# Kernel tuning notes

Measured on AMD Instinct MI355X. Metric: run time of the kernel, lower is better.

The kernel has to match this reference:

```python
import jax, jax.numpy as jnp
import numpy as np

N = 4096      # num_nodes
B = 32        # batch
U = 64        # num_units
L = 2         # num_rnn_layers
K = 2         # max_diffusion_step
OUT = 1       # output_dim (also decoder input_dim)
NM = 2 * K + 1  # num_matrices: 2 supports * K cheb steps + identity


def _random_walk_T(adj):
    # calculate_random_walk_matrix(adj).T : (D^-1 W)^T
    d = adj.sum(axis=1)
    return (adj / d[:, None]).T


def setup_inputs():
    key = jax.random.key(0)
    ks = jax.random.split(key, 16)
    adj = jax.random.uniform(ks[0], (N, N), dtype=jnp.float32)
    S_fwd = _random_walk_T(adj)      # forward transition, transposed
    S_bwd = _random_walk_T(adj.T)    # backward transition, transposed

    inputs = jax.random.normal(ks[1], (B, N, OUT), dtype=jnp.float32)
    hidden_state = jax.random.normal(ks[2], (L, B, N, U), dtype=jnp.float32) * 0.1

    D0 = OUT + U   # layer 0 gconv input width
    D1 = U + U     # layer 1 gconv input width
    s = 0.05
    Wg0 = jax.random.normal(ks[3], (NM * D0, 2 * U), jnp.float32) * s
    bg0 = jnp.ones((2 * U,), jnp.float32)          # bias_start = 1.0 for gates
    Wc0 = jax.random.normal(ks[4], (NM * D0, U), jnp.float32) * s
    bc0 = jnp.zeros((U,), jnp.float32)
    Wg1 = jax.random.normal(ks[5], (NM * D1, 2 * U), jnp.float32) * s
    bg1 = jnp.ones((2 * U,), jnp.float32)
    Wc1 = jax.random.normal(ks[6], (NM * D1, U), jnp.float32) * s
    bc1 = jnp.zeros((U,), jnp.float32)
    Wp = jax.random.normal(ks[7], (U, OUT), jnp.float32) * s
    bp = jnp.zeros((OUT,), jnp.float32)
    return {
        "inputs": inputs, "hidden_state": hidden_state,
        "S_fwd": S_fwd, "S_bwd": S_bwd,
        "Wg0": Wg0, "bg0": bg0, "Wc0": Wc0, "bc0": bc0,
        "Wg1": Wg1, "bg1": bg1, "Wc1": Wc1, "bc1": bc1,
        "Wp": Wp, "bp": bp,
    }


def _gconv(supports, x, h, W, b):
    # diffusion graph convolution with Chebyshev recursion (DCRNN)
    x0 = jnp.concatenate([x, h], axis=-1)      # (B, N, D)
    xs = [x0]
    for S in supports:
        x1 = jnp.einsum('mn,bnd->bmd', S, x0)
        xs.append(x1)
        xk_2, xk_1 = x0, x1
        for _ in range(K - 1):
            x2 = 2.0 * jnp.einsum('mn,bnd->bmd', S, xk_1) - xk_2
            xs.append(x2)
            xk_2, xk_1 = xk_1, x2
    X = jnp.concatenate(xs, axis=-1)           # (B, N, NM*D)
    return X @ W + b


def _dcgru_cell(supports, x, h, Wg, bg, Wc, bc):
    value = jax.nn.sigmoid(_gconv(supports, x, h, Wg, bg))   # (B, N, 2U)
    r, u = jnp.split(value, 2, axis=-1)
    c = jnp.tanh(_gconv(supports, x, r * h, Wc, bc))
    return u * h + (1.0 - u) * c


def reference(inputs, hidden_state, S_fwd, S_bwd,
              Wg0, bg0, Wc0, bc0, Wg1, bg1, Wc1, bc1, Wp, bp):
    supports = (S_fwd, S_bwd)
    layer_params = [(Wg0, bg0, Wc0, bc0), (Wg1, bg1, Wc1, bc1)]
    out = inputs
    new_hidden = []
    for i, (Wg, bg, Wc, bc) in enumerate(layer_params):
        h = _dcgru_cell(supports, out, hidden_state[i], Wg, bg, Wc, bc)
        new_hidden.append(h)
        out = h
    predict = out @ Wp + bp                    # (B, N, OUT)
    return predict, jnp.stack(new_hidden)
```

## Files before the change

### kernel.cpp

```cpp
#include <hip/hip_runtime.h>

typedef unsigned short u16;
typedef unsigned int u32;
typedef unsigned long long u64;
typedef short v8s __attribute__((ext_vector_type(8)));
typedef float v4f __attribute__((ext_vector_type(4)));

#define NN 4096
#define BATCH 32

__device__ __forceinline__ float b2f(u16 u) {
  union { u32 i; float f; } c; c.i = ((u32)u) << 16; return c.f;
}
__device__ __forceinline__ u16 f2b(float f) {
  union { float f; u32 i; } c; c.f = f;
  u32 x = c.i;
  return (u16)((x + 0x7fffu + ((x >> 16) & 1u)) >> 16);
}
__device__ __forceinline__ u32 pk2(float a, float b) {
  return (u32)f2b(a) | ((u32)f2b(b) << 16);
}

typedef const __attribute__((address_space(1))) u32* gp_t;
typedef __attribute__((address_space(3))) u32* lp_t;
__device__ __forceinline__ void gld16(const u16* g, u16* l) {
  __builtin_amdgcn_global_load_lds((gp_t)g, (lp_t)l, 16, 0, 0);
}

#define CBAR() asm volatile("" ::: "memory")
#define BARRIER() do { CBAR(); __builtin_amdgcn_s_barrier(); CBAR(); } while (0)
#define LGKM0() asm volatile("s_waitcnt lgkmcnt(0)" ::: "memory")
#define VMC4() asm volatile("s_waitcnt vmcnt(4)" ::: "memory")
#define VMC0() asm volatile("s_waitcnt vmcnt(0)" ::: "memory")

__global__ __launch_bounds__(256) void cvtS(const float* __restrict__ S,
                                            u16* __restrict__ Sb) {
  const u64 idx = ((u64)blockIdx.x * 256 + threadIdx.x) * 8;
  const float4 a = *(const float4*)(S + idx);
  const float4 b = *(const float4*)(S + idx + 4);
  uint4 o;
  o.x = pk2(a.x, a.y); o.y = pk2(a.z, a.w);
  o.z = pk2(b.x, b.y); o.w = pk2(b.z, b.w);
  *(uint4*)(Sb + idx) = o;
}

__global__ __launch_bounds__(512, 2) void gemm256(const u16* __restrict__ A,
                                                  const u16* __restrict__ B,
                                                  u16* __restrict__ Ct,
                                                  const u16* __restrict__ Xt) {
  __shared__ __align__(16) u16 lds[65536];
  const int t = threadIdx.x;
  const int wave = t >> 6, lane = t & 63;
  const int q = lane >> 4, r16 = lane & 15;
  const int wm = wave >> 2, wn = wave & 3;

  const int nwg = (int)(gridDim.x * gridDim.y);
  const int bid = (int)(blockIdx.y * gridDim.x + blockIdx.x);
  const int swz = (bid & 7) * (nwg >> 3) + (bid >> 3);
  const int m0 = (swz & 15) << 8;
  const int c0 = (swz >> 4) << 8;

  v4f acc[8][4];
  const v4f vz = {0.f, 0.f, 0.f, 0.f};
#pragma unroll
  for (int i = 0; i < 8; ++i)
#pragma unroll
    for (int j = 0; j < 4; ++j) acc[i][j] = vz;

  const int srow = t >> 3;
  const int sslot = ((t & 7) ^ (srow & 7)) << 3;
  const u16* pA = A + (u64)(m0 + srow) * NN + sslot;
  const u16* pB = B + (u64)(c0 + srow) * NN + sslot;
  const u64 rstep = (u64)64 * NN;
  const u64 hstep = (u64)128 * NN;
  u16* lw = lds + (wave << 9);

  const int sw8 = (q ^ (r16 & 7)) << 3;
  const int aBase = (wm << 13) + (r16 << 6) + sw8;
  const int bBase = 16384 + ((wn >> 1) << 13) + ((wn & 1) << 12) + (r16 << 6) + sw8;

  const int NT = NN >> 6;

  gld16(pA, lw);
  gld16(pA + rstep, lw + 4096);
  gld16(pA + hstep, lw + 8192);
  gld16(pA + hstep + rstep, lw + 12288);
  gld16(pB, lw + 16384);
  gld16(pB + rstep, lw + 20480);
  gld16(pB + hstep, lw + 24576);
  gld16(pB + hstep + rstep, lw + 28672);
  gld16(pB + 64, lw + 32768 + 16384);
  gld16(pB + 64 + rstep, lw + 32768 + 20480);
  gld16(pB + 64 + hstep, lw + 32768 + 24576);
  gld16(pB + 64 + hstep + rstep, lw + 32768 + 28672);
  VMC4();
  BARRIER();

  v8s af[4][2], bf01[2][2], bf23[2][2];
#pragma unroll
  for (int i = 0; i < 4; ++i) {
    const int a = aBase + (i << 10);
    af[i][0] = *(const v8s*)(lds + a);
    af[i][1] = *(const v8s*)(lds + (a ^ 32));
  }
#pragma unroll
  for (int j = 0; j < 2; ++j) {
    const int b = bBase + (j << 10);
    bf01[j][0] = *(const v8s*)(lds + b);
    bf01[j][1] = *(const v8s*)(lds + (b ^ 32));
  }

#pragma unroll 2
  for (int T = 0; T < NT; ++T) {
    const int bo = (T & 1) << 15;
    const int no = bo ^ 32768;
    const u64 ka = (u64)(T + 1 < NT ? T + 1 : NT - 1) << 6;
    const u64 kb = (u64)(T + 2 < NT ? T + 2 : NT - 1) << 6;

    gld16(pA + ka, lw + no);
    gld16(pA + ka + rstep, lw + no + 4096);
#pragma unroll
    for (int j = 0; j < 2; ++j) {
      const int b = bo + bBase + ((2 + j) << 10);
      bf23[j][0] = *(const v8s*)(lds + b);
      bf23[j][1] = *(const v8s*)(lds + (b ^ 32));
    }
    __builtin_amdgcn_s_setprio(1);
#pragma unroll
    for (int i = 0; i < 4; ++i)
#pragma unroll
      for (int j = 0; j < 2; ++j) {
        acc[i][j] = __builtin_amdgcn_mfma_f32_16x16x32_bf16(af[i][0], bf01[j][0], acc[i][j], 0, 0, 0);
        acc[i][j] = __builtin_amdgcn_mfma_f32_16x16x32_bf16(af[i][1], bf01[j][1], acc[i][j], 0, 0, 0);
      }
    __builtin_amdgcn_s_setprio(0);

    gld16(pA + hstep + ka, lw + no + 8192);
    gld16(pA + hstep + ka + rstep, lw + no + 12288);
    LGKM0();
    BARRIER();
    __builtin_amdgcn_s_setprio(1);
#pragma unroll
    for (int i = 0; i < 4; ++i)
#pragma unroll
      for (int j = 0; j < 2; ++j) {
        acc[i][2 + j] = __builtin_amdgcn_mfma_f32_16x16x32_bf16(af[i][0], bf23[j][0], acc[i][2 + j], 0, 0, 0);
        acc[i][2 + j] = __builtin_amdgcn_mfma_f32_16x16x32_bf16(af[i][1], bf23[j][1], acc[i][2 + j], 0, 0, 0);
      }
    __builtin_amdgcn_s_setprio(0);
#pragma unroll
    for (int i = 0; i < 4; ++i) {
      const int a = bo + aBase + ((4 + i) << 10);
      af[i][0] = *(const v8s*)(lds + a);
      af[i][1] = *(const v8s*)(lds + (a ^ 32));
    }
    __builtin_amdgcn_sched_barrier(0);

    gld16(pB + kb, lw + bo + 16384);
    gld16(pB + kb + rstep, lw + bo + 20480);
    __builtin_amdgcn_s_setprio(1);
#pragma unroll
    for (int i = 0; i < 4; ++i)
#pragma unroll
      for (int j = 0; j < 2; ++j) {
        acc[4 + i][2 + j] = __builtin_amdgcn_mfma_f32_16x16x32_bf16(af[i][0], bf23[j][0], acc[4 + i][2 + j], 0, 0, 0);
        acc[4 + i][2 + j] = __builtin_amdgcn_mfma_f32_16x16x32_bf16(af[i][1], bf23[j][1], acc[4 + i][2 + j], 0, 0, 0);
      }
    __builtin_amdgcn_s_setprio(0);

    gld16(pB + hstep + kb, lw + bo + 24576);
    gld16(pB + hstep + kb + rstep, lw + bo + 28672);
    VMC4();
    BARRIER();
    __builtin_amdgcn_s_setprio(1);
#pragma unroll
    for (int i = 0; i < 4; ++i)
#pragma unroll
      for (int j = 0; j < 2; ++j) {
        acc[4 + i][j] = __builtin_amdgcn_mfma_f32_16x16x32_bf16(af[i][0], bf01[j][0], acc[4 + i][j], 0, 0, 0);
        acc[4 + i][j] = __builtin_amdgcn_mfma_f32_16x16x32_bf16(af[i][1], bf01[j][1], acc[4 + i][j], 0, 0, 0);
      }
    __builtin_amdgcn_s_setprio(0);
#pragma unroll
    for (int i = 0; i < 4; ++i) {
      const int a = no + aBase + (i << 10);
      af[i][0] = *(const v8s*)(lds + a);
      af[i][1] = *(const v8s*)(lds + (a ^ 32));
    }
#pragma unroll
    for (int j = 0; j < 2; ++j) {
      const int b = no + bBase + (j << 10);
      bf01[j][0] = *(const v8s*)(lds + b);
      bf01[j][1] = *(const v8s*)(lds + (b ^ 32));
    }
    __builtin_amdgcn_sched_barrier(0);
  }

  VMC0();
  __syncthreads();
#pragma unroll
  for (int i = 0; i < 8; ++i)
#pragma unroll
    for (int j = 0; j < 4; ++j) {
      const int cl = (wn << 6) + (j << 4) + r16;
      const int ml = (wm << 7) + (i << 4) + (q << 2);
      const int phys = (cl << 8) + ((((ml >> 3) ^ (cl & 7)) << 3) | (ml & 7));
      uint2 pv;
      pv.x = pk2(acc[i][j][0], acc[i][j][1]);
      pv.y = pk2(acc[i][j][2], acc[i][j][3]);
      *(uint2*)(lds + phys) = pv;
    }
  __syncthreads();
#pragma unroll
  for (int it = 0; it < 16; ++it) {
    const int f = (it << 9) + t;
    const int cl = f >> 5, sl = f & 31;
    const int phys = (cl << 8) + ((sl ^ (cl & 7)) << 3);
    union { uint4 v; u16 e[8]; } tv;
    tv.v = *(const uint4*)(lds + phys);
    const u64 gi = (u64)(c0 + cl) * NN + m0 + (sl << 3);
    if (Xt) {
      union { uint4 v; u16 e[8]; } xv, ov;
      xv.v = *(const uint4*)(Xt + gi);
#pragma unroll
      for (int s = 0; s < 8; ++s) ov.e[s] = f2b(2.f * b2f(tv.e[s]) - b2f(xv.e[s]));
      *(uint4*)(Ct + gi) = ov.v;
    } else {
      *(uint4*)(Ct + gi) = tv.v;
    }
  }
}

__global__ __launch_bounds__(256) void gemm_s(const float* __restrict__ A,
                                              const u16* __restrict__ B,
                                              u16* __restrict__ Ct,
                                              const u16* __restrict__ Xt) {
  __shared__ __align__(16) u16 As[4096];
  __shared__ __align__(16) u16 Bs[4096];
  __shared__ __align__(16) u16 T[16384];
  const int t = threadIdx.x;
  const int wave = t >> 6, lane = t & 63;
  const int m0 = blockIdx.x << 7, c0 = blockIdx.y << 7;
  const int wm = (wave >> 1) << 6, wc = (wave & 1) << 6;
  const int q = lane >> 4, r16 = lane & 15;
  v4f acc[4][4];
  const v4f vz = {0.f, 0.f, 0.f, 0.f};
#pragma unroll
  for (int i = 0; i < 4; ++i)
#pragma unroll
    for (int j = 0; j < 4; ++j) acc[i][j] = vz;

  const int sr = t >> 2;
  const int sc = (t & 3) << 3;
  const u64 abase = (u64)(m0 + sr) * NN + sc;
  const u64 bbase = (u64)(c0 + sr) * NN + sc;
  const u64 rstep = (u64)64 * NN;
  u16* as0 = As + sr * 32 + sc;
  u16* as1 = As + (64 + sr) * 32 + sc;
  u16* bs0 = Bs + sr * 32 + sc;
  u16* bs1 = Bs + (64 + sr) * 32 + sc;

  for (int k0 = 0; k0 < NN; k0 += 32) {
    const float4 a0l = *(const float4*)(A + abase + k0);
    const float4 a0h = *(const float4*)(A + abase + k0 + 4);
    const float4 a1l = *(const float4*)(A + abase + rstep + k0);
    const float4 a1h = *(const float4*)(A + abase + rstep + k0 + 4);
    const uint4 b0 = *(const uint4*)(B + bbase + k0);
    const uint4 b1 = *(const uint4*)(B + bbase + rstep + k0);
    uint4 pa0, pa1;
    pa0.x = pk2(a0l.x, a0l.y); pa0.y = pk2(a0l.z, a0l.w);
    pa0.z = pk2(a0h.x, a0h.y); pa0.w = pk2(a0h.z, a0h.w);
    pa1.x = pk2(a1l.x, a1l.y); pa1.y = pk2(a1l.z, a1l.w);
    pa1.z = pk2(a1h.x, a1h.y); pa1.w = pk2(a1h.z, a1h.w);
    __syncthreads();
    *(uint4*)as0 = pa0;
    *(uint4*)as1 = pa1;
    *(uint4*)bs0 = b0;
    *(uint4*)bs1 = b1;
    __syncthreads();
    v8s af[4], bf[4];
#pragma unroll
    for (int i = 0; i < 4; ++i)
      af[i] = *(const v8s*)(As + ((wm + i * 16 + r16) << 5) + (q << 3));
#pragma unroll
    for (int j = 0; j < 4; ++j)
      bf[j] = *(const v8s*)(Bs + ((wc + j * 16 + r16) << 5) + (q << 3));
#pragma unroll
    for (int i = 0; i < 4; ++i)
#pragma unroll
      for (int j = 0; j < 4; ++j)
        acc[i][j] = __builtin_amdgcn_mfma_f32_16x16x32_bf16(af[i], bf[j], acc[i][j], 0, 0, 0);
  }
#pragma unroll
  for (int i = 0; i < 4; ++i)
#pragma unroll
    for (int j = 0; j < 4; ++j) {
      const int cl = wc + j * 16 + r16;
      const int mm = wm + i * 16 + (q << 2);
      uint2 pv;
      pv.x = pk2(acc[i][j][0], acc[i][j][1]);
      pv.y = pk2(acc[i][j][2], acc[i][j][3]);
      *(uint2*)(T + (cl << 7) + mm) = pv;
    }
  __syncthreads();
#pragma unroll
  for (int it = 0; it < 8; ++it) {
    const int flat = it * 256 + t;
    const int cl = flat >> 4;
    const int seg = (flat & 15) << 3;
    const u64 gi = (u64)(c0 + cl) * NN + m0 + seg;
    union { uint4 v; u16 e[8]; } tv;
    tv.v = *(uint4*)(T + (cl << 7) + seg);
    if (Xt) {
      union { uint4 v; u16 e[8]; } xv, ov;
      xv.v = *(const uint4*)(Xt + gi);
#pragma unroll
      for (int s = 0; s < 8; ++s) ov.e[s] = f2b(2.f * b2f(tv.e[s]) - b2f(xv.e[s]));
      *(uint4*)(Ct + gi) = ov.v;
    } else {
      *(uint4*)(Ct + gi) = tv.v;
    }
  }
}

template <int DP, int KTOT>
__global__ __launch_bounds__(256) void proj_k(const u16* __restrict__ Wt,
                                              const u16* __restrict__ F,
                                              const float* __restrict__ bias,
                                              u16* __restrict__ outp,
                                              const int JSTR, const int ACT) {
  __shared__ __align__(16) u16 As2[2048];
  __shared__ __align__(16) u16 Bs2[4096];
  const int t = threadIdx.x;
  const int wave = t >> 6, lane = t & 63;
  const int q = lane >> 4, r16 = lane & 15;
  const int n0 = blockIdx.x << 7;
  const int j0 = blockIdx.y << 6;
  const int b = blockIdx.z;
  v4f acc[4][2];
  const v4f vz = {0.f, 0.f, 0.f, 0.f};
#pragma unroll
  for (int i = 0; i < 4; ++i) { acc[i][0] = vz; acc[i][1] = vz; }

  const int ar = t >> 2, ac = (t & 3) << 3;
  const u64 wbase = (u64)(j0 + ar) * KTOT + ac;

  for (int k0 = 0; k0 < KTOT; k0 += 32) {
    const uint4 av = *(const uint4*)(Wt + wbase + k0);
    uint4 bv[2];
#pragma unroll
    for (int ci = 0; ci < 2; ++ci) {
      const int c = ci * 256 + t;
      const int kr = c >> 4;
      const int seg = (c & 15) << 3;
      const int kk = k0 + kr;
      const int i = kk / DP;
      const int d = kk - i * DP;
      bv[ci] = *(const uint4*)(F + ((u64)i * (BATCH * DP) + (u64)b * DP + d) * NN + n0 + seg);
    }
    __syncthreads();
    *(uint4*)(As2 + ar * 32 + ac) = av;
#pragma unroll
    for (int ci = 0; ci < 2; ++ci) {
      const int c = ci * 256 + t;
      const int kr = c >> 4;
      const int seg = (c & 15) << 3;
      *(uint4*)(Bs2 + (kr << 7) + seg) = bv[ci];
    }
    __syncthreads();
    v8s af[4], bf[2];
#pragma unroll
    for (int i = 0; i < 4; ++i)
      af[i] = *(const v8s*)(As2 + ((i * 16 + r16) << 5) + (q << 3));
#pragma unroll
    for (int jj = 0; jj < 2; ++jj) {
      const int nn = (wave << 5) + jj * 16 + r16;
      v8s v;
#pragma unroll
      for (int s = 0; s < 8; ++s) v[s] = (short)Bs2[(((q << 3) + s) << 7) + nn];
      bf[jj] = v;
    }
#pragma unroll
    for (int i = 0; i < 4; ++i)
#pragma unroll
      for (int jj = 0; jj < 2; ++jj)
        acc[i][jj] = __builtin_amdgcn_mfma_f32_16x16x32_bf16(af[i], bf[jj], acc[i][jj], 0, 0, 0);
  }
#pragma unroll
  for (int i = 0; i < 4; ++i)
#pragma unroll
    for (int jj = 0; jj < 2; ++jj)
#pragma unroll
      for (int r = 0; r < 4; ++r) {
        const int j = j0 + i * 16 + (q << 2) + r;
        const int n = n0 + (wave << 5) + jj * 16 + r16;
        float v = acc[i][jj][r] + bias[j];
        v = ACT ? (1.f - 2.f / (__expf(2.f * v) + 1.f)) : (1.f / (1.f + __expf(-v)));
        outp[((u64)b * JSTR + j) * NN + n] = f2b(v);
      }
}

__global__ __launch_bounds__(256) void repackW(const float* __restrict__ W, u16* __restrict__ Wt,
                                               const int D, const int DP, const int KTOT,
                                               const int J) {
  const int idx = blockIdx.x * 256 + threadIdx.x;
  if (idx >= J * KTOT) return;
  const int j = idx / KTOT, k = idx - j * KTOT;
  const int i = k / DP, d = k - i * DP;
  u16 v = 0;
  if (i < 5 && d < D) v = f2b(W[(i * D + d) * J + j]);
  Wt[idx] = v;
}

__global__ __launch_bounds__(256) void pack0(const float* __restrict__ x,
                                             const float* __restrict__ hid0,
                                             u16* __restrict__ F0) {
  __shared__ __align__(16) u16 Hs[64 * 72];
  const int b = blockIdx.y, n0 = blockIdx.x << 6, t = threadIdx.x;
  const int r = t >> 2, ds = t & 3;
  const float* hrow = hid0 + ((u64)b * NN + n0 + r) * 64;
#pragma unroll
  for (int c4 = 0; c4 < 4; ++c4) {
    const float4 v = *(const float4*)(hrow + ds * 16 + c4 * 4);
    uint2 p;
    p.x = pk2(v.x, v.y);
    p.y = pk2(v.z, v.w);
    *(uint2*)(Hs + r * 72 + ds * 16 + c4 * 4) = p;
  }
  __syncthreads();
#pragma unroll
  for (int c2 = 0; c2 < 2; ++c2) {
    union { uint4 v; u16 h[8]; } o;
#pragma unroll
    for (int s = 0; s < 8; ++s) o.h[s] = Hs[(ds * 16 + c2 * 8 + s) * 72 + r];
    *(uint4*)(F0 + ((u64)b * 72 + 1 + r) * NN + n0 + ds * 16 + c2 * 8) = o.v;
  }
  if (t < 64) {
    F0[(u64)b * 72 * NN + n0 + t] = f2b(x[(u64)b * NN + n0 + t]);
  } else if (t < 120) {
    const int tt = t - 64;
    const int row = 65 + (tt >> 3), seg = (tt & 7) << 3;
    uint4 z; z.x = z.y = z.z = z.w = 0;
    *(uint4*)(F0 + ((u64)b * 72 + row) * NN + n0 + seg) = z;
  }
}

__global__ __launch_bounds__(256) void pack1(const float* __restrict__ hid1,
                                             u16* __restrict__ F1) {
  __shared__ __align__(16) u16 Hs[64 * 72];
  const int b = blockIdx.y, n0 = blockIdx.x << 6, t = threadIdx.x;
  const int r = t >> 2, ds = t & 3;
  const float* hrow = hid1 + ((u64)b * NN + n0 + r) * 64;
#pragma unroll
  for (int c4 = 0; c4 < 4; ++c4) {
    const float4 v = *(const float4*)(hrow + ds * 16 + c4 * 4);
    uint2 p;
    p.x = pk2(v.x, v.y);
    p.y = pk2(v.z, v.w);
    *(uint2*)(Hs + r * 72 + ds * 16 + c4 * 4) = p;
  }
  __syncthreads();
#pragma unroll
  for (int c2 = 0; c2 < 2; ++c2) {
    union { uint4 v; u16 h[8]; } o;
#pragma unroll
    for (int s = 0; s < 8; ++s) o.h[s] = Hs[(ds * 16 + c2 * 8 + s) * 72 + r];
    *(uint4*)(F1 + ((u64)b * 128 + 64 + r) * NN + n0 + ds * 16 + c2 * 8) = o.v;
  }
}

__global__ __launch_bounds__(256) void candpack(const u16* __restrict__ G, u16* __restrict__ F,
                                                const int DP, const int OFF) {
  const int u = blockIdx.x * 256 + threadIdx.x;
  const int b = u >> 15;
  const int d = (u >> 9) & 63;
  const int seg = (u & 511) << 3;
  union { uint4 v; u16 h[8]; } g, f, o;
  g.v = *(const uint4*)(G + ((u64)b * 128 + d) * NN + seg);
  u16* fp = F + ((u64)b * DP + OFF + d) * NN + seg;
  f.v = *(const uint4*)fp;
#pragma unroll
  for (int s = 0; s < 8; ++s) o.h[s] = f2b(b2f(f.h[s]) * b2f(g.h[s]));
  *(uint4*)fp = o.v;
}

__global__ __launch_bounds__(256) void hnew_k(const u16* __restrict__ G,
                                              const float* __restrict__ hidL,
                                              u16* __restrict__ HnF,
                                              float* __restrict__ outH) {
  __shared__ __align__(16) float Hs[64 * 72];
  __shared__ __align__(16) float T2[64 * 72];
  const int b = blockIdx.y, n0 = blockIdx.x << 6, t = threadIdx.x;
  const int r = t >> 2, ds = t & 3;
  const float* hrow = hidL + ((u64)b * NN + n0 + r) * 64;
#pragma unroll
  for (int c4 = 0; c4 < 4; ++c4)
    *(float4*)(Hs + r * 72 + ds * 16 + c4 * 4) = *(const float4*)(hrow + ds * 16 + c4 * 4);
  __syncthreads();
#pragma unroll
  for (int c2 = 0; c2 < 2; ++c2) {
    const int ncol = ds * 16 + c2 * 8;
    union { uint4 v; u16 h[8]; } uv, cv, o;
    uv.v = *(const uint4*)(G + ((u64)b * 128 + 64 + r) * NN + n0 + ncol);
    cv.v = *(const uint4*)(G + ((u64)b * 128 + r) * NN + n0 + ncol);
#pragma unroll
    for (int s = 0; s < 8; ++s) {
      const int nl = ncol + s;
      const float uu = b2f(uv.h[s]);
      const float hh = Hs[nl * 72 + r];
      const float cc = b2f(cv.h[s]);
      const float v = uu * hh + (1.f - uu) * cc;
      o.h[s] = f2b(v);
      T2[nl * 72 + r] = v;
    }
    *(uint4*)(HnF + ((u64)b * 128 + r) * NN + n0 + ncol) = o.v;
  }
  __syncthreads();
  const int nl2 = t >> 2, dseg = (t & 3) << 4;
#pragma unroll
  for (int c4 = 0; c4 < 4; ++c4) {
    const float4 v = *(const float4*)(T2 + nl2 * 72 + dseg + c4 * 4);
    *(float4*)(outH + ((u64)b * NN + n0 + nl2) * 64 + dseg + c4 * 4) = v;
  }
}

__global__ __launch_bounds__(256) void predictk(const float* __restrict__ H1bnd,
                                                const float* __restrict__ Wp,
                                                const float* __restrict__ bp,
                                                float* __restrict__ outp) {
  __shared__ float w[64];
  __shared__ float bb;
  const int t = threadIdx.x;
  if (t < 64) w[t] = Wp[t];
  if (t == 64) bb = bp[0];
  __syncthreads();
  const int idx = blockIdx.x * 256 + t;
  const float* h = H1bnd + (u64)idx * 64;
  float acc = bb;
#pragma unroll
  for (int c4 = 0; c4 < 16; ++c4) {
    const float4 v = *(const float4*)(h + c4 * 4);
    acc += v.x * w[c4 * 4] + v.y * w[c4 * 4 + 1] + v.z * w[c4 * 4 + 2] + v.w * w[c4 * 4 + 3];
  }
  outp[idx] = acc;
}

static inline void launch_gemm(bool big, const float* Af, const u16* Ab,
                               const u16* B, u16* Ct, const u16* Xt,
                               int Cdim, hipStream_t s) {
  if (big) gemm256<<<dim3(16, Cdim >> 8), 512, 0, s>>>(Ab, B, Ct, Xt);
  else     gemm_s<<<dim3(32, Cdim >> 7), 256, 0, s>>>(Af, B, Ct, Xt);
}

extern "C" void kernel_launch(void* const* d_in, const int* in_sizes, int n_in,
                              void* d_out, int out_size, void* d_ws, size_t ws_size,
                              hipStream_t stream) {
  const float* X   = (const float*)d_in[0];
  const float* HID = (const float*)d_in[1];
  const float* Sf  = (const float*)d_in[2];
  const float* Sb  = (const float*)d_in[3];
  const float* Wg0 = (const float*)d_in[4];
  const float* bg0 = (const float*)d_in[5];
  const float* Wc0 = (const float*)d_in[6];
  const float* bc0 = (const float*)d_in[7];
  const float* Wg1 = (const float*)d_in[8];
  const float* bg1 = (const float*)d_in[9];
  const float* Wc1 = (const float*)d_in[10];
  const float* bc1 = (const float*)d_in[11];
  const float* Wp  = (const float*)d_in[12];
  const float* bp  = (const float*)d_in[13];
  float* OUT = (float*)d_out;
  char* ws = (char*)d_ws;

  u16* F = (u16*)(ws);
  u16* G = (u16*)(ws + 167772160ull);
  const u64 NEED_BIG = 167772160ull + 33554432ull + 2ull * 33554432ull + 393216ull;
  const bool big = ws_size >= NEED_BIG;
  u16* Sfb = (u16*)(ws + 167772160ull + 33554432ull);
  u16* Sbb = Sfb + (u64)NN * NN;
  u16* WT = big ? (Sbb + (u64)NN * NN)
                : (u16*)(ws + 167772160ull + 33554432ull);
  u16* Wg0t = WT;
  u16* Wc0t = Wg0t + 128 * 384;
  u16* Wg1t = Wc0t + 64 * 384;
  u16* Wc1t = Wg1t + 128 * 640;

  const float* HID1 = HID + (u64)32 * 4096 * 64;
  float* OUT_H0 = OUT + 131072;
  float* OUT_H1 = OUT + 131072 + 8388608;

  hipMemsetAsync(ws + (u64)11520 * NN * 2, 0, (u64)2304 * NN * 2, stream);

  if (big) {
    cvtS<<<8192, 256, 0, stream>>>(Sf, Sfb);
    cvtS<<<8192, 256, 0, stream>>>(Sb, Sbb);
  }

  repackW<<<(128 * 384 + 255) / 256, 256, 0, stream>>>(Wg0, Wg0t, 65, 72, 384, 128);
  repackW<<<(64 * 384 + 255) / 256, 256, 0, stream>>>(Wc0, Wc0t, 65, 72, 384, 64);
  repackW<<<(128 * 640 + 255) / 256, 256, 0, stream>>>(Wg1, Wg1t, 128, 128, 640, 128);
  repackW<<<(64 * 640 + 255) / 256, 256, 0, stream>>>(Wc1, Wc1t, 128, 128, 640, 64);

  pack0<<<dim3(64, 32), 256, 0, stream>>>(X, HID, F);
  const u64 R0 = (u64)2304 * NN;
  launch_gemm(big, Sf, Sfb, F, F + R0, nullptr, 2304, stream);
  launch_gemm(big, Sb, Sbb, F, F + 3 * R0, nullptr, 2304, stream);
  launch_gemm(big, Sf, Sfb, F + R0, F + 2 * R0, F, 2304, stream);
  launch_gemm(big, Sb, Sbb, F + 3 * R0, F + 4 * R0, F, 2304, stream);
  proj_k<72, 384><<<dim3(32, 2, 32), 256, 0, stream>>>(Wg0t, F, bg0, G, 128, 0);
  candpack<<<4096, 256, 0, stream>>>(G, F, 72, 1);
  launch_gemm(big, Sf, Sfb, F, F + R0, nullptr, 2304, stream);
  launch_gemm(big, Sb, Sbb, F, F + 3 * R0, nullptr, 2304, stream);
  launch_gemm(big, Sf, Sfb, F + R0, F + 2 * R0, F, 2304, stream);
  launch_gemm(big, Sb, Sbb, F + 3 * R0, F + 4 * R0, F, 2304, stream);
  proj_k<72, 384><<<dim3(32, 1, 32), 256, 0, stream>>>(Wc0t, F, bc0, G, 128, 1);
  hnew_k<<<dim3(64, 32), 256, 0, stream>>>(G, HID, F, OUT_H0);

  pack1<<<dim3(64, 32), 256, 0, stream>>>(HID1, F);
  const u64 R1 = (u64)4096 * NN;
  launch_gemm(big, Sf, Sfb, F, F + R1, nullptr, 4096, stream);
  launch_gemm(big, Sb, Sbb, F, F + 3 * R1, nullptr, 4096, stream);
  launch_gemm(big, Sf, Sfb, F + R1, F + 2 * R1, F, 4096, stream);
  launch_gemm(big, Sb, Sbb, F + 3 * R1, F + 4 * R1, F, 4096, stream);
  proj_k<128, 640><<<dim3(32, 2, 32), 256, 0, stream>>>(Wg1t, F, bg1, G, 128, 0);
  candpack<<<4096, 256, 0, stream>>>(G, F, 128, 64);
  launch_gemm(big, Sf, Sfb, F, F + R1, nullptr, 4096, stream);
  launch_gemm(big, Sb, Sbb, F, F + 3 * R1, nullptr, 4096, stream);
  launch_gemm(big, Sf, Sfb, F + R1, F + 2 * R1, F, 4096, stream);
  launch_gemm(big, Sb, Sbb, F + 3 * R1, F + 4 * R1, F, 4096, stream);
  proj_k<128, 640><<<dim3(32, 1, 32), 256, 0, stream>>>(Wc1t, F, bc1, G, 128, 1);
  hnew_k<<<dim3(64, 32), 256, 0, stream>>>(G, HID1, F, OUT_H1);

  predictk<<<512, 256, 0, stream>>>(OUT_H1, Wp, bp, OUT);
}
```

Measured before the change: 1.991 ms.

## Add 128x256 double-buffered GEMM fusing forward/backward supports for layer 0

Adds a new 512-thread bf16 MFMA GEMM kernel with 128x256 tiles, LDS double buffering with staggered A/B staging, priority hints and workgroup swizzling. It also batches the forward and backward support products into one launch through the z grid dimension. The kernel replaces the four per-layer-0 diffusion GEMM launches with two, cutting launch count and improving reuse and occupancy of the S-matrix tiles. Layer 1 still uses the old path, and the N=2304 column count must divide evenly into 256-wide tiles (9 tiles).

```diff
diff --git a/kernel.cpp b/kernel.cpp
--- a/kernel.cpp
+++ b/kernel.cpp
@@ -227,6 +227,171 @@
       *(uint4*)(Ct + gi) = ov.v;
     } else {
       *(uint4*)(Ct + gi) = tv.v;
+    }
+  }
+}
+
+__global__ __launch_bounds__(512, 2) void gemm_h(const u16* __restrict__ A0f,
+                                                 const u16* __restrict__ A1f,
+                                                 const u16* __restrict__ B0f,
+                                                 const u16* __restrict__ B1f,
+                                                 u16* __restrict__ C0f,
+                                                 u16* __restrict__ C1f,
+                                                 const u16* __restrict__ Xt) {
+  __shared__ __align__(16) u16 lds[49152];
+  const int t = threadIdx.x;
+  const int wave = t >> 6, lane = t & 63;
+  const int q = lane >> 4, r16 = lane & 15;
+  const int wm = wave >> 2, wn = wave & 3;
+  const int z = blockIdx.z;
+  const u16* A = z ? A1f : A0f;
+  const u16* B = z ? B1f : B0f;
+  u16* C = z ? C1f : C0f;
+
+  const int nwg = (int)(gridDim.x * gridDim.y);
+  const int bid = (int)(blockIdx.y * gridDim.x + blockIdx.x);
+  const int swz = (bid & 7) * (nwg >> 3) + (bid >> 3);
+  const int m0 = (swz & 31) << 7;
+  const int c0 = (swz >> 5) << 8;
+
+  v4f acc[4][4];
+  const v4f vz = {0.f, 0.f, 0.f, 0.f};
+#pragma unroll
+  for (int i = 0; i < 4; ++i)
+#pragma unroll
+    for (int j = 0; j < 4; ++j) acc[i][j] = vz;
+
+  const int srow = t >> 3;
+  const int sslot = ((t & 7) ^ (srow & 7)) << 3;
+  const u16* pA = A + (u64)(m0 + srow) * NN + sslot;
+  const u16* pB = B + (u64)(c0 + srow) * NN + sslot;
+  const u64 rstep = (u64)64 * NN;
+  u16* lw = lds + (wave << 9);
+
+  const int sw8 = (q ^ (r16 & 7)) << 3;
+  const int aBase = (wm << 12) + (r16 << 6) + sw8;
+  const int bBase = 8192 + (wn << 12) + (r16 << 6) + sw8;
+
+  const int NT = NN >> 6;
+
+#define STAGE_A(bufo, koff)                        \
+  do {                                             \
+    gld16(pA + (koff), lw + (bufo));               \
+    gld16(pA + rstep + (koff), lw + (bufo) + 4096);\
+  } while (0)
+#define STAGE_B(bufo, koff)                                    \
+  do {                                                         \
+    gld16(pB + (koff), lw + (bufo) + 8192);                    \
+    gld16(pB + rstep + (koff), lw + (bufo) + 12288);           \
+    gld16(pB + 2 * rstep + (koff), lw + (bufo) + 16384);       \
+    gld16(pB + 3 * rstep + (koff), lw + (bufo) + 20480);       \
+  } while (0)
+
+  STAGE_A(0, 0);
+  STAGE_B(0, 0);
+  STAGE_B(24576, 64);
+  VMC4();
+  BARRIER();
+
+  v8s af[4][2], bf01[2][2], bf23[2][2];
+#pragma unroll
+  for (int i = 0; i < 4; ++i) {
+    const int a = aBase + (i << 10);
+    af[i][0] = *(const v8s*)(lds + a);
+    af[i][1] = *(const v8s*)(lds + (a ^ 32));
+  }
+#pragma unroll
+  for (int j = 0; j < 2; ++j) {
+    const int b = bBase + (j << 10);
+    bf01[j][0] = *(const v8s*)(lds + b);
+    bf01[j][1] = *(const v8s*)(lds + (b ^ 32));
+  }
+
+  for (int T = 0; T < NT; ++T) {
+    const int bo = (T & 1) ? 24576 : 0;
+    const int no = bo ^ 24576;
+    const u64 ka = (u64)(T + 1 < NT ? T + 1 : NT - 1) << 6;
+    const u64 kb = (u64)(T + 2 < NT ? T + 2 : NT - 1) << 6;
+
+    STAGE_A(no, ka);
+#pragma unroll
+    for (int j = 0; j < 2; ++j) {
+      const int b = bo + bBase + ((2 + j) << 10);
+      bf23[j][0] = *(const v8s*)(lds + b);
+      bf23[j][1] = *(const v8s*)(lds + (b ^ 32));
+    }
+    __builtin_amdgcn_s_setprio(1);
+#pragma unroll
+    for (int i = 0; i < 4; ++i)
+#pragma unroll
+      for (int j = 0; j < 2; ++j) {
+        acc[i][j] = __builtin_amdgcn_mfma_f32_16x16x32_bf16(af[i][0], bf01[j][0], acc[i][j], 0, 0, 0);
+        acc[i][j] = __builtin_amdgcn_mfma_f32_16x16x32_bf16(af[i][1], bf01[j][1], acc[i][j], 0, 0, 0);
+      }
+    __builtin_amdgcn_s_setprio(0);
+    LGKM0();
+    BARRIER();
+
+    STAGE_B(bo, kb);
+    VMC4();
+    BARRIER();
+    __builtin_amdgcn_s_setprio(1);
+#pragma unroll
+    for (int i = 0; i < 4; ++i)
+#pragma unroll
+      for (int j = 0; j < 2; ++j) {
+        acc[i][2 + j] = __builtin_amdgcn_mfma_f32_16x16x32_bf16(af[i][0], bf23[j][0], acc[i][2 + j], 0, 0, 0);
+        acc[i][2 + j] = __builtin_amdgcn_mfma_f32_16x16x32_bf16(af[i][1], bf23[j][1], acc[i][2 + j], 0, 0, 0);
+      }
+    __builtin_amdgcn_s_setprio(0);
+#pragma unroll
+    for (int i = 0; i < 4; ++i) {
+      const int a = no + aBase + (i << 10);
+      af[i][0] = *(const v8s*)(lds + a);
+      af[i][1] = *(const v8s*)(lds + (a ^ 32));
+    }
+#pragma unroll
+    for (int j = 0; j < 2; ++j) {
+      const int b = no + bBase + (j << 10);
+      bf01[j][0] = *(const v8s*)(lds + b);
+      bf01[j][1] = *(const v8s*)(lds + (b ^ 32));
+    }
+    __builtin_amdgcn_sched_barrier(0);
+  }
+#undef STAGE_A
+#undef STAGE_B
+
+  VMC0();
+  __syncthreads();
+#pragma unroll
+  for (int i = 0; i < 4; ++i)
+#pragma unroll
+    for (int j = 0; j < 4; ++j) {
+      const int cl = (wn << 6) + (j << 4) + r16;
+      const int slot = (wm << 3) + (i << 1) + (q >> 1);
+      const int phys = (cl << 7) + ((slot ^ (cl & 7)) << 3) + ((q & 1) << 2);
+      uint2 pv;
+      pv.x = pk2(acc[i][j][0], acc[i][j][1]);
+      pv.y = pk2(acc[i][j][2], acc[i][j][3]);
+      *(uint2*)(lds + phys) = pv;
+    }
+  __syncthreads();
+#pragma unroll
+  for (int it = 0; it < 8; ++it) {
+    const int f = (it << 9) + t;
+    const int cl = f >> 4, sl = f & 15;
+    const int phys = (cl << 7) + ((sl ^ (cl & 7)) << 3);
+    union { uint4 v; u16 e[8]; } tv;
+    tv.v = *(const uint4*)(lds + phys);
+    const u64 gi = (u64)(c0 + cl) * NN + m0 + (sl << 3);
+    if (Xt) {
+      union { uint4 v; u16 e[8]; } xv, ov;
+      xv.v = *(const uint4*)(Xt + gi);
+#pragma unroll
+      for (int s = 0; s < 8; ++s) ov.e[s] = f2b(2.f * b2f(tv.e[s]) - b2f(xv.e[s]));
+      *(uint4*)(C + gi) = ov.v;
+    } else {
+      *(uint4*)(C + gi) = tv.v;
     }
   }
 }
@@ -603,16 +768,27 @@
 
   pack0<<<dim3(64, 32), 256, 0, stream>>>(X, HID, F);
   const u64 R0 = (u64)2304 * NN;
-  launch_gemm(big, Sf, Sfb, F, F + R0, nullptr, 2304, stream);
-  launch_gemm(big, Sb, Sbb, F, F + 3 * R0, nullptr, 2304, stream);
-  launch_gemm(big, Sf, Sfb, F + R0, F + 2 * R0, F, 2304, stream);
-  launch_gemm(big, Sb, Sbb, F + 3 * R0, F + 4 * R0, F, 2304, stream);
+  const dim3 gh(32, 9, 2);
+  if (big) {
+    gemm_h<<<gh, 512, 0, stream>>>(Sfb, Sbb, F, F, F + R0, F + 3 * R0, nullptr);
+    gemm_h<<<gh, 512, 0, stream>>>(Sfb, Sbb, F + R0, F + 3 * R0, F + 2 * R0, F + 4 * R0, F);
+  } else {
+    launch_gemm(big, Sf, Sfb, F, F + R0, nullptr, 2304, stream);
+    launch_gemm(big, Sb, Sbb, F, F + 3 * R0, nullptr, 2304, stream);
+    launch_gemm(big, Sf, Sfb, F + R0, F + 2 * R0, F, 2304, stream);
+    launch_gemm(big, Sb, Sbb, F + 3 * R0, F + 4 * R0, F, 2304, stream);
+  }
   proj_k<72, 384><<<dim3(32, 2, 32), 256, 0, stream>>>(Wg0t, F, bg0, G, 128, 0);
   candpack<<<4096, 256, 0, stream>>>(G, F, 72, 1);
-  launch_gemm(big, Sf, Sfb, F, F + R0, nullptr, 2304, stream);
-  launch_gemm(big, Sb, Sbb, F, F + 3 * R0, nullptr, 2304, stream);
-  launch_gemm(big, Sf, Sfb, F + R0, F + 2 * R0, F, 2304, stream);
-  launch_gemm(big, Sb, Sbb, F + 3 * R0, F + 4 * R0, F, 2304, stream);
+  if (big) {
+    gemm_h<<<gh, 512, 0, stream>>>(Sfb, Sbb, F, F, F + R0, F + 3 * R0, nullptr);
+    gemm_h<<<gh, 512, 0, stream>>>(Sfb, Sbb, F + R0, F + 3 * R0, F + 2 * R0, F + 4 * R0, F);
+  } else {
+    launch_gemm(big, Sf, Sfb, F, F + R0, nullptr, 2304, stream);
+    launch_gemm(big, Sb, Sbb, F, F + 3 * R0, nullptr, 2304, stream);
+    launch_gemm(big, Sf, Sfb, F + R0, F + 2 * R0, F, 2304, stream);
+    launch_gemm(big, Sb, Sbb, F + 3 * R0, F + 4 * R0, F, 2304, stream);
+  }
   proj_k<72, 384><<<dim3(32, 1, 32), 256, 0, stream>>>(Wc0t, F, bc0, G, 128, 1);
   hnew_k<<<dim3(64, 32), 256, 0, stream>>>(G, HID, F, OUT_H0);
 
```

Measured after the change: 2.056 ms. 3.3% more time.
